# Kernel tuning notes

Measured on AMD Instinct MI355X. Metric: run time of the kernel, lower is better.

## Reference

```python
import jax, jax.numpy as jnp
import numpy as np
from jax import lax

DIM = 256
NUM_HEADS = 8
HEAD_DIM = DIM // NUM_HEADS          # 32
KEY_DIM = int(HEAD_DIM * 0.5)        # 16
SCALE = KEY_DIM ** -0.5
H_QKV = DIM + KEY_DIM * NUM_HEADS * 2  # 512
BN_EPS = 1e-3  # keras BatchNormalization default epsilon


def conv_bn(x, w, gamma, beta, mean, var, groups=1):
    # Conv2D (no bias) + BatchNorm (inference), activation=None
    y = lax.conv_general_dilated(
        x, w, window_strides=(1, 1), padding='SAME',
        dimension_numbers=('NHWC', 'HWIO', 'NHWC'),
        feature_group_count=groups)
    return gamma * (y - mean) * lax.rsqrt(var + BN_EPS) + beta


def setup_inputs() -> dict:
    key = jax.random.key(0)
    ks = jax.random.split(key, 4)
    B, Hs, Ws = 8, 32, 32
    inp = {
        'inputs': jax.random.normal(ks[0], (B, Hs, Ws, DIM), dtype=jnp.float32),
        # qkv: 1x1 conv dim -> h
        'qkv_w': jax.random.normal(ks[1], (1, 1, DIM, H_QKV), dtype=jnp.float32) * 0.05,
        'qkv_gamma': jnp.ones((H_QKV,), jnp.float32),
        'qkv_beta': jnp.zeros((H_QKV,), jnp.float32),
        'qkv_mean': jnp.zeros((H_QKV,), jnp.float32),
        'qkv_var': jnp.ones((H_QKV,), jnp.float32),
        # pe: 3x3 depthwise conv (groups=dim)
        'pe_w': jax.random.normal(ks[2], (3, 3, 1, DIM), dtype=jnp.float32) * 0.05,
        'pe_gamma': jnp.ones((DIM,), jnp.float32),
        'pe_beta': jnp.zeros((DIM,), jnp.float32),
        'pe_mean': jnp.zeros((DIM,), jnp.float32),
        'pe_var': jnp.ones((DIM,), jnp.float32),
        # proj: 1x1 conv dim -> dim
        'proj_w': jax.random.normal(ks[3], (1, 1, DIM, DIM), dtype=jnp.float32) * 0.05,
        'proj_gamma': jnp.ones((DIM,), jnp.float32),
        'proj_beta': jnp.zeros((DIM,), jnp.float32),
        'proj_mean': jnp.zeros((DIM,), jnp.float32),
        'proj_var': jnp.ones((DIM,), jnp.float32),
    }
    return inp


def reference(inputs, qkv_w, qkv_gamma, qkv_beta, qkv_mean, qkv_var,
              pe_w, pe_gamma, pe_beta, pe_mean, pe_var,
              proj_w, proj_gamma, proj_beta, proj_mean, proj_var):
    B, Hs, Ws, C = inputs.shape
    N = Hs * Ws
    x = conv_bn(inputs, qkv_w, qkv_gamma, qkv_beta, qkv_mean, qkv_var)  # [B,H,W,h]
    x = x.reshape(B, N, NUM_HEADS, 2 * KEY_DIM + HEAD_DIM)
    q = x[..., :KEY_DIM]                          # [B,N,nh,kd]
    k = x[..., KEY_DIM:2 * KEY_DIM]               # [B,N,nh,kd]
    v = x[..., 2 * KEY_DIM:]                      # [B,N,nh,hd]
    # attn = q^T @ k^T : [B,nh,N,N]
    attn = jnp.einsum('bnhk,bmhk->bhnm', q, k) * SCALE
    attn = jax.nn.softmax(attn, axis=-1)
    # x = v^T @ attn : [B,nh,hd,N]
    x = jnp.einsum('bnhd,bhnm->bhdm', v, attn)
    # faithful to source: transpose [0,2,1,3] -> [B,hd,nh,N], then reshape NHWC
    x = jnp.transpose(x, (0, 2, 1, 3)).reshape(B, Hs, Ws, C)
    pe = conv_bn(v.reshape(B, Hs, Ws, C), pe_w, pe_gamma, pe_beta, pe_mean, pe_var, groups=C)
    x = x + pe
    x = conv_bn(x, proj_w, proj_gamma, proj_beta, proj_mean, proj_var)
    return x
```

## Files before the change

### kernel.cpp

```cpp
#include <hip/hip_runtime.h>

typedef _Float16 h4 __attribute__((ext_vector_type(4)));
typedef _Float16 h8 __attribute__((ext_vector_type(8)));
typedef float    f4 __attribute__((ext_vector_type(4)));

#define QSCALE (0.25f * 1.44269504088896f)

__device__ __forceinline__ float ex2(float x){ return __builtin_amdgcn_exp2f(x); }

__global__ __launch_bounds__(256) void prep_k(
    const float* __restrict__ X,
    const float* __restrict__ qkvw, const float* __restrict__ qg, const float* __restrict__ qb,
    const float* __restrict__ qm,   const float* __restrict__ qv,
    const float* __restrict__ pew,  const float* __restrict__ pg, const float* __restrict__ pb,
    const float* __restrict__ pm,   const float* __restrict__ pv,
    const float* __restrict__ prw,  const float* __restrict__ prg, const float* __restrict__ prb,
    const float* __restrict__ prm,  const float* __restrict__ prv,
    _Float16* __restrict__ Xh, _Float16* __restrict__ Wqkv, float* __restrict__ bqkv,
    _Float16* __restrict__ Wproj, float* __restrict__ bproj,
    float* __restrict__ peW, float* __restrict__ peB)
{
  const int gid = blockIdx.x*256 + threadIdx.x;
  const int gsz = gridDim.x*256;
  for (int i = gid; i < 2097152/4; i += gsz){
    const float4 xv = ((const float4*)X)[i];
    h4 o; o[0]=(_Float16)xv.x; o[1]=(_Float16)xv.y; o[2]=(_Float16)xv.z; o[3]=(_Float16)xv.w;
    ((h4*)Xh)[i] = o;
  }
  for (int i = gid; i < 512*256; i += gsz){
    int o = i >> 8, c = i & 255;
    float s = qg[o] * rsqrtf(qv[o] + 1e-3f);
    Wqkv[i] = (_Float16)(qkvw[c*512 + o] * s);
  }
  for (int i = gid; i < 512; i += gsz){
    float s = qg[i] * rsqrtf(qv[i] + 1e-3f);
    bqkv[i] = qb[i] - qm[i]*s;
  }
  for (int i = gid; i < 256*256; i += gsz){
    int o = i >> 8, c = i & 255;
    float s = prg[o] * rsqrtf(prv[o] + 1e-3f);
    Wproj[i] = (_Float16)(prw[c*256 + o] * s);
  }
  for (int i = gid; i < 256; i += gsz){
    float s = prg[i] * rsqrtf(prv[i] + 1e-3f);
    bproj[i] = prb[i] - prm[i]*s;
  }
  for (int i = gid; i < 9*256; i += gsz){
    int c = i & 255;
    float s = pg[c] * rsqrtf(pv[c] + 1e-3f);
    peW[i] = pew[i] * s;
  }
  for (int i = gid; i < 256; i += gsz){
    float s = pg[i] * rsqrtf(pv[i] + 1e-3f);
    peB[i] = pb[i] - pm[i]*s;
  }
}

template<int EPI, int MT>
__global__ __launch_bounds__(256) void gemm_staged_k(
    const _Float16* __restrict__ A, const _Float16* __restrict__ Bt,
    const float* __restrict__ bias,
    _Float16* __restrict__ Qh, _Float16* __restrict__ Kh, _Float16* __restrict__ Vh,
    float* __restrict__ Out)
{
  constexpr int BM = MT*32;
  constexpr int AR = BM/64;
  __shared__ __align__(16) _Float16 As[BM*40];
  __shared__ __align__(16) _Float16 Bs[64*40];
  const int t = threadIdx.x, lane = t & 63, wv = t >> 6;
  const int l15 = lane & 15, q = lane >> 4;
  const int wr = wv & 1, wc = wv >> 1;
  const int m0 = blockIdx.x*BM, n0 = blockIdx.y*64;
  const int r4 = t >> 2, s4 = t & 3;
  uint4 ar[AR], br;
  #pragma unroll
  for (int i = 0; i < AR; ++i)
    ar[i] = *(const uint4*)(A + (size_t)(m0 + r4 + i*64)*256 + s4*8);
  br = *(const uint4*)(Bt + (size_t)(n0 + r4)*256 + s4*8);
  f4 acc[MT][2] = {};
  #pragma unroll
  for (int kk = 0; kk < 8; ++kk){
    #pragma unroll
    for (int i = 0; i < AR; ++i)
      *(uint4*)&As[(r4 + i*64)*40 + s4*8] = ar[i];
    *(uint4*)&Bs[r4*40 + s4*8] = br;
    __syncthreads();
    if (kk < 7){
      #pragma unroll
      for (int i = 0; i < AR; ++i)
        ar[i] = *(const uint4*)(A + (size_t)(m0 + r4 + i*64)*256 + (kk+1)*32 + s4*8);
      br = *(const uint4*)(Bt + (size_t)(n0 + r4)*256 + (kk+1)*32 + s4*8);
    }
    #pragma unroll
    for (int mi = 0; mi < MT; ++mi){
      h8 af = *(const h8*)&As[(wr*(MT*16) + mi*16 + l15)*40 + q*8];
      #pragma unroll
      for (int nj = 0; nj < 2; ++nj){
        h8 bf = *(const h8*)&Bs[(wc*32 + nj*16 + l15)*40 + q*8];
        acc[mi][nj] = __builtin_amdgcn_mfma_f32_16x16x32_f16(af, bf, acc[mi][nj], 0,0,0);
      }
    }
    __syncthreads();
  }
  #pragma unroll
  for (int mi = 0; mi < MT; ++mi)
  #pragma unroll
  for (int nj = 0; nj < 2; ++nj){
    const int og = n0 + wc*32 + nj*16 + l15;
    const float bs = bias[og];
    #pragma unroll
    for (int r = 0; r < 4; ++r){
      const int mg = m0 + wr*(MT*16) + mi*16 + q*4 + r;
      const float v = acc[mi][nj][r] + bs;
      if (EPI == 0){
        const int h = og >> 6, j = og & 63;
        const int b = mg >> 10, n = mg & 1023;
        const size_t bhn = (size_t)(b*8+h)*1024 + n;
        if (j < 16)      Qh[bhn*16 + j]      = (_Float16)(v * QSCALE);
        else if (j < 32) Kh[bhn*16 + (j-16)] = (_Float16)v;
        else             Vh[bhn*32 + (j-32)] = (_Float16)v;
      } else {
        Out[(size_t)mg*256 + og] = v;
      }
    }
  }
}

__global__ __launch_bounds__(256) void pass1_k(
    const _Float16* __restrict__ Qh, const _Float16* __restrict__ Kh,
    const _Float16* __restrict__ Vh, _Float16* __restrict__ Vs)
{
  __shared__ __align__(16) _Float16 Ks[64*24];
  const int t = threadIdx.x, lane = t & 63, wv = t >> 6;
  const int l15 = lane & 15, q = lane >> 4;
  const int bh = blockIdx.y;
  const int n0 = (blockIdx.x*4 + wv) * 32;
  const size_t qb = (size_t)bh*1024;
  const h4 af0 = *(const h4*)(Qh + (qb + n0 + l15)*16 + q*4);
  const h4 af1 = *(const h4*)(Qh + (qb + n0 + 16 + l15)*16 + q*4);
  f4 sm0 = {0.f,0.f,0.f,0.f}, sm1 = {0.f,0.f,0.f,0.f};
  const _Float16* kp = Kh + qb*16;
  const int sr = t >> 1, ss = t & 1;
  uint4 kr;
  if (t < 128) kr = *(const uint4*)(kp + sr*16 + ss*8);
  for (int mt = 0; mt < 1024; mt += 64){
    if (t < 128) *(uint4*)&Ks[sr*24 + ss*8] = kr;
    __syncthreads();
    if (t < 128 && mt + 64 < 1024)
      kr = *(const uint4*)(kp + (mt + 64 + sr)*16 + ss*8);
    #pragma unroll
    for (int sub = 0; sub < 4; ++sub){
      h4 bf = *(const h4*)&Ks[(sub*16 + l15)*24 + q*4];
      f4 z = {0.f,0.f,0.f,0.f};
      f4 d0 = __builtin_amdgcn_mfma_f32_16x16x16f16(af0, bf, z, 0,0,0);
      f4 d1 = __builtin_amdgcn_mfma_f32_16x16x16f16(af1, bf, z, 0,0,0);
      #pragma unroll
      for (int r = 0; r < 4; ++r){ sm0[r] += ex2(d0[r]); sm1[r] += ex2(d1[r]); }
    }
    __syncthreads();
  }
  #pragma unroll
  for (int st = 1; st < 16; st <<= 1){
    #pragma unroll
    for (int r = 0; r < 4; ++r){
      sm0[r] += __shfl_xor(sm0[r], st, 64);
      sm1[r] += __shfl_xor(sm1[r], st, 64);
    }
  }
  f4 cv0, cv1;
  #pragma unroll
  for (int r = 0; r < 4; ++r){ cv0[r] = 1.0f/sm0[r]; cv1[r] = 1.0f/sm1[r]; }
  #pragma unroll
  for (int half = 0; half < 2; ++half){
    const int dd = l15 + half*16;
    h4 o0, o1;
    #pragma unroll
    for (int r = 0; r < 4; ++r){
      o0[r] = (_Float16)((float)Vh[(qb + n0 + q*4 + r)*32 + dd] * cv0[r]);
      o1[r] = (_Float16)((float)Vh[(qb + n0 + 16 + q*4 + r)*32 + dd] * cv1[r]);
    }
    *(h4*)(Vs + ((size_t)bh*32 + dd)*1024 + n0 + q*4)      = o0;
    *(h4*)(Vs + ((size_t)bh*32 + dd)*1024 + n0 + 16 + q*4) = o1;
  }
}

__global__ __launch_bounds__(256) void pass2_k(
    const _Float16* __restrict__ Qh, const _Float16* __restrict__ Kh,
    const _Float16* __restrict__ Vs, _Float16* __restrict__ X1h)
{
  __shared__ __align__(16) _Float16 Qs[64*24];
  __shared__ __align__(16) _Float16 Vss[32*72];
  __shared__ float Tt[4][32*33];
  const int t = threadIdx.x, lane = t & 63, wv = t >> 6;
  const int l15 = lane & 15, q = lane >> 4;
  const int bh = blockIdx.y;
  const int b  = bh >> 3, h = bh & 7;
  const int mb = (blockIdx.x*4 + wv) * 32;
  const size_t qb = (size_t)bh*1024;
  const h4 kf0 = *(const h4*)(Kh + (qb + mb + l15)*16 + q*4);
  const h4 kf1 = *(const h4*)(Kh + (qb + mb + 16 + l15)*16 + q*4);
  const _Float16* qp = Qh + qb*16;
  const _Float16* vp = Vs + (size_t)bh*32*1024;
  const int sr = t >> 1, ss = t & 1;
  const int vd = t >> 3, vc = (t & 7)*8;
  uint4 qr, vr;
  if (t < 128) qr = *(const uint4*)(qp + sr*16 + ss*8);
  vr = *(const uint4*)(vp + (size_t)vd*1024 + vc);
  f4 a00={0.f,0.f,0.f,0.f}, a01={0.f,0.f,0.f,0.f};
  f4 a10={0.f,0.f,0.f,0.f}, a11={0.f,0.f,0.f,0.f};
  for (int nt = 0; nt < 1024; nt += 64){
    if (t < 128) *(uint4*)&Qs[sr*24 + ss*8] = qr;
    *(uint4*)&Vss[vd*72 + vc] = vr;
    __syncthreads();
    if (nt + 64 < 1024){
      if (t < 128) qr = *(const uint4*)(qp + (nt + 64 + sr)*16 + ss*8);
      vr = *(const uint4*)(vp + (size_t)vd*1024 + nt + 64 + vc);
    }
    #pragma unroll
    for (int sub = 0; sub < 4; ++sub){
      h4 qf = *(const h4*)&Qs[(sub*16 + l15)*24 + q*4];
      h4 b0 = *(const h4*)&Vss[l15*72      + sub*16 + q*4];
      h4 b1 = *(const h4*)&Vss[(16+l15)*72 + sub*16 + q*4];
      f4 z = {0.f,0.f,0.f,0.f};
      f4 s0 = __builtin_amdgcn_mfma_f32_16x16x16f16(qf, kf0, z, 0,0,0);
      f4 s1 = __builtin_amdgcn_mfma_f32_16x16x16f16(qf, kf1, z, 0,0,0);
      h4 p0, p1;
      #pragma unroll
      for (int r = 0; r < 4; ++r){ p0[r] = (_Float16)ex2(s0[r]); p1[r] = (_Float16)ex2(s1[r]); }
      a00 = __builtin_amdgcn_mfma_f32_16x16x16f16(p0, b0, a00, 0,0,0);
      a01 = __builtin_amdgcn_mfma_f32_16x16x16f16(p0, b1, a01, 0,0,0);
      a10 = __builtin_amdgcn_mfma_f32_16x16x16f16(p1, b0, a10, 0,0,0);
      a11 = __builtin_amdgcn_mfma_f32_16x16x16f16(p1, b1, a11, 0,0,0);
    }
    __syncthreads();
  }
  #pragma unroll
  for (int r = 0; r < 4; ++r){
    Tt[wv][(q*4 + r)*33      + l15]      = a00[r];
    Tt[wv][(q*4 + r)*33      + 16 + l15] = a01[r];
    Tt[wv][(16 + q*4 + r)*33 + l15]      = a10[r];
    Tt[wv][(16 + q*4 + r)*33 + 16 + l15] = a11[r];
  }
  __syncthreads();
  _Float16* xb = X1h + (size_t)b*262144 + (size_t)h*1024 + mb;
  const int mloc = lane & 31, dh = lane >> 5;
  #pragma unroll
  for (int r = 0; r < 16; ++r){
    const int d = r*2 + dh;
    xb[(size_t)d*8192 + mloc] = (_Float16)Tt[wv][mloc*33 + d];
  }
}

__global__ __launch_bounds__(256) void pe_add_k(
    const _Float16* __restrict__ Vh, const _Float16* __restrict__ X1h,
    const float* __restrict__ peW, const float* __restrict__ peB,
    _Float16* __restrict__ X2h)
{
  const int u = blockIdx.x*256 + threadIdx.x;
  const int c0 = (u & 31) * 8;
  const int tok = u >> 5;
  const int b = tok >> 10, n = tok & 1023;
  const int hs = n >> 5, ws = n & 31;
  const int h = c0 >> 5, d0 = c0 & 31;
  const size_t idx8 = (size_t)tok*256 + c0;
  float acc[8];
  {
    f4 b0v = *(const f4*)(peB + c0), b1v = *(const f4*)(peB + c0 + 4);
    #pragma unroll
    for (int j = 0; j < 4; ++j){ acc[j] = b0v[j]; acc[4+j] = b1v[j]; }
  }
  const _Float16* vb = Vh + (size_t)(b*8 + h)*32768 + d0;
  #pragma unroll
  for (int dy = 0; dy < 3; ++dy){
    const int y = hs + dy - 1;
    if ((unsigned)y < 32u){
      #pragma unroll
      for (int dx = 0; dx < 3; ++dx){
        const int x = ws + dx - 1;
        if ((unsigned)x < 32u){
          const int kk = dy*3 + dx;
          h8 vv = *(const h8*)(vb + (size_t)(y*32 + x)*32);
          f4 w0 = *(const f4*)(peW + kk*256 + c0);
          f4 w1 = *(const f4*)(peW + kk*256 + c0 + 4);
          #pragma unroll
          for (int j = 0; j < 4; ++j){
            acc[j]   += w0[j] * (float)vv[j];
            acc[4+j] += w1[j] * (float)vv[4+j];
          }
        }
      }
    }
  }
  h8 x1 = *(const h8*)(X1h + idx8);
  h8 o;
  #pragma unroll
  for (int j = 0; j < 8; ++j) o[j] = (_Float16)((float)x1[j] + acc[j]);
  *(h8*)(X2h + idx8) = o;
}

extern "C" void kernel_launch(void* const* d_in, const int* in_sizes, int n_in,
                              void* d_out, int out_size, void* d_ws, size_t ws_size,
                              hipStream_t stream)
{
  const float* X    = (const float*)d_in[0];
  const float* qkvw = (const float*)d_in[1];
  const float* qg   = (const float*)d_in[2];
  const float* qb   = (const float*)d_in[3];
  const float* qm   = (const float*)d_in[4];
  const float* qv   = (const float*)d_in[5];
  const float* pew  = (const float*)d_in[6];
  const float* pg   = (const float*)d_in[7];
  const float* pb   = (const float*)d_in[8];
  const float* pm   = (const float*)d_in[9];
  const float* pv   = (const float*)d_in[10];
  const float* prw  = (const float*)d_in[11];
  const float* prg  = (const float*)d_in[12];
  const float* prb  = (const float*)d_in[13];
  const float* prm  = (const float*)d_in[14];
  const float* prv  = (const float*)d_in[15];

  char* ws = (char*)d_ws;
  _Float16* Xh    = (_Float16*)(ws + 0);
  _Float16* X2h   = (_Float16*)(ws + 0);
  _Float16* Qh    = (_Float16*)(ws + 4194304);
  _Float16* Kh    = (_Float16*)(ws + 6291456);
  _Float16* Vh    = (_Float16*)(ws + 8388608);
  _Float16* Vs    = (_Float16*)(ws + 12582912);
  _Float16* X1h   = (_Float16*)(ws + 16777216);
  _Float16* Wqkv  = (_Float16*)(ws + 20971520);
  float*    bqkv  = (float*)   (ws + 21233664);
  _Float16* Wproj = (_Float16*)(ws + 21235712);
  float*    bproj = (float*)   (ws + 21366784);
  float*    peW   = (float*)   (ws + 21367808);
  float*    peB   = (float*)   (ws + 21377024);

  prep_k<<<512, 256, 0, stream>>>(X, qkvw, qg, qb, qm, qv, pew, pg, pb, pm, pv,
                                  prw, prg, prb, prm, prv,
                                  Xh, Wqkv, bqkv, Wproj, bproj, peW, peB);
  gemm_staged_k<0,4><<<dim3(64, 8), 256, 0, stream>>>(Xh, Wqkv, bqkv,
                                                      Qh, Kh, Vh, nullptr);
  pass1_k<<<dim3(8, 64), 256, 0, stream>>>(Qh, Kh, Vh, Vs);
  pass2_k<<<dim3(8, 64), 256, 0, stream>>>(Qh, Kh, Vs, X1h);
  pe_add_k<<<1024, 256, 0, stream>>>(Vh, X1h, peW, peB, X2h);
  gemm_staged_k<1,2><<<dim3(128, 4), 256, 0, stream>>>(X2h, Wproj, bproj,
                                                       nullptr, nullptr, nullptr,
                                                       (float*)d_out);
}
```

Baseline: 150.8 us.

## Fuse input fp16 cast into QKV GEMM and stage whole K/Q per block

The fp32-to-fp16 conversion of the input moves out of the prep kernel and into a new QKV GEMM that loads fp32 X directly, removing a full write and re-read of the converted activations. Both GEMMs become 64x64 tiles with two 128-wide K chunks, in place of eight 32-wide steps. pass1 now loads all 1024 keys for a head into shared memory once, so the per-tile barriers go away. pass2 preloads all Q into LDS and streams V in 256-column chunks. The cost is much larger shared-memory use per block (about 40-57 KB), which may lower occupancy.

```diff
diff --git a/kernel.cpp b/kernel.cpp
--- a/kernel.cpp
+++ b/kernel.cpp
@@ -9,24 +9,18 @@
 __device__ __forceinline__ float ex2(float x){ return __builtin_amdgcn_exp2f(x); }
 
 __global__ __launch_bounds__(256) void prep_k(
-    const float* __restrict__ X,
     const float* __restrict__ qkvw, const float* __restrict__ qg, const float* __restrict__ qb,
     const float* __restrict__ qm,   const float* __restrict__ qv,
     const float* __restrict__ pew,  const float* __restrict__ pg, const float* __restrict__ pb,
     const float* __restrict__ pm,   const float* __restrict__ pv,
     const float* __restrict__ prw,  const float* __restrict__ prg, const float* __restrict__ prb,
     const float* __restrict__ prm,  const float* __restrict__ prv,
-    _Float16* __restrict__ Xh, _Float16* __restrict__ Wqkv, float* __restrict__ bqkv,
+    _Float16* __restrict__ Wqkv, float* __restrict__ bqkv,
     _Float16* __restrict__ Wproj, float* __restrict__ bproj,
     float* __restrict__ peW, float* __restrict__ peB)
 {
   const int gid = blockIdx.x*256 + threadIdx.x;
   const int gsz = gridDim.x*256;
-  for (int i = gid; i < 2097152/4; i += gsz){
-    const float4 xv = ((const float4*)X)[i];
-    h4 o; o[0]=(_Float16)xv.x; o[1]=(_Float16)xv.y; o[2]=(_Float16)xv.z; o[3]=(_Float16)xv.w;
-    ((h4*)Xh)[i] = o;
-  }
   for (int i = gid; i < 512*256; i += gsz){
     int o = i >> 8, c = i & 255;
     float s = qg[o] * rsqrtf(qv[o] + 1e-3f);
@@ -56,72 +50,156 @@
   }
 }
 
-template<int EPI, int MT>
-__global__ __launch_bounds__(256) void gemm_staged_k(
-    const _Float16* __restrict__ A, const _Float16* __restrict__ Bt,
+__global__ __launch_bounds__(256) void qkv_gemm_k(
+    const float* __restrict__ X, const _Float16* __restrict__ Wqkv,
     const float* __restrict__ bias,
-    _Float16* __restrict__ Qh, _Float16* __restrict__ Kh, _Float16* __restrict__ Vh,
-    float* __restrict__ Out)
-{
-  constexpr int BM = MT*32;
-  constexpr int AR = BM/64;
-  __shared__ __align__(16) _Float16 As[BM*40];
-  __shared__ __align__(16) _Float16 Bs[64*40];
+    _Float16* __restrict__ Qh, _Float16* __restrict__ Kh, _Float16* __restrict__ Vh)
+{
+  __shared__ __align__(16) _Float16 As[64*136];
+  __shared__ __align__(16) _Float16 Bs[64*136];
   const int t = threadIdx.x, lane = t & 63, wv = t >> 6;
   const int l15 = lane & 15, q = lane >> 4;
   const int wr = wv & 1, wc = wv >> 1;
-  const int m0 = blockIdx.x*BM, n0 = blockIdx.y*64;
-  const int r4 = t >> 2, s4 = t & 3;
-  uint4 ar[AR], br;
-  #pragma unroll
-  for (int i = 0; i < AR; ++i)
-    ar[i] = *(const uint4*)(A + (size_t)(m0 + r4 + i*64)*256 + s4*8);
-  br = *(const uint4*)(Bt + (size_t)(n0 + r4)*256 + s4*8);
-  f4 acc[MT][2] = {};
-  #pragma unroll
-  for (int kk = 0; kk < 8; ++kk){
-    #pragma unroll
-    for (int i = 0; i < AR; ++i)
-      *(uint4*)&As[(r4 + i*64)*40 + s4*8] = ar[i];
-    *(uint4*)&Bs[r4*40 + s4*8] = br;
-    __syncthreads();
-    if (kk < 7){
-      #pragma unroll
-      for (int i = 0; i < AR; ++i)
-        ar[i] = *(const uint4*)(A + (size_t)(m0 + r4 + i*64)*256 + (kk+1)*32 + s4*8);
-      br = *(const uint4*)(Bt + (size_t)(n0 + r4)*256 + (kk+1)*32 + s4*8);
-    }
-    #pragma unroll
-    for (int mi = 0; mi < MT; ++mi){
-      h8 af = *(const h8*)&As[(wr*(MT*16) + mi*16 + l15)*40 + q*8];
-      #pragma unroll
-      for (int nj = 0; nj < 2; ++nj){
-        h8 bf = *(const h8*)&Bs[(wc*32 + nj*16 + l15)*40 + q*8];
-        acc[mi][nj] = __builtin_amdgcn_mfma_f32_16x16x32_f16(af, bf, acc[mi][nj], 0,0,0);
+  const int m0 = blockIdx.x*64, n0 = blockIdx.y*64;
+  const int ar = t >> 2, ac = t & 3;
+  float4 av[8]; uint4 bv[4];
+  #pragma unroll
+  for (int i = 0; i < 8; ++i){
+    int idx = i*256 + t, row = idx >> 5, c4 = idx & 31;
+    av[i] = *(const float4*)(X + (size_t)(m0+row)*256 + c4*4);
+  }
+  #pragma unroll
+  for (int i = 0; i < 4; ++i){
+    int idx = i*256 + t, row = idx >> 4, seg = idx & 15;
+    bv[i] = *(const uint4*)(Wqkv + (size_t)(n0+row)*256 + seg*8);
+  }
+  f4 acc[2][2] = {};
+  #pragma unroll
+  for (int kc = 0; kc < 2; ++kc){
+    #pragma unroll
+    for (int i = 0; i < 8; ++i){
+      int idx = i*256 + t, row = idx >> 5, c4 = idx & 31;
+      h4 o; o[0]=(_Float16)av[i].x; o[1]=(_Float16)av[i].y;
+            o[2]=(_Float16)av[i].z; o[3]=(_Float16)av[i].w;
+      *(h4*)&As[row*136 + c4*4] = o;
+    }
+    #pragma unroll
+    for (int i = 0; i < 4; ++i){
+      int idx = i*256 + t, row = idx >> 4, seg = idx & 15;
+      *(uint4*)&Bs[row*136 + seg*8] = bv[i];
+    }
+    __syncthreads();
+    if (kc == 0){
+      #pragma unroll
+      for (int i = 0; i < 8; ++i){
+        int idx = i*256 + t, row = idx >> 5, c4 = idx & 31;
+        av[i] = *(const float4*)(X + (size_t)(m0+row)*256 + 128 + c4*4);
       }
-    }
-    __syncthreads();
-  }
-  #pragma unroll
-  for (int mi = 0; mi < MT; ++mi)
+      #pragma unroll
+      for (int i = 0; i < 4; ++i){
+        int idx = i*256 + t, row = idx >> 4, seg = idx & 15;
+        bv[i] = *(const uint4*)(Wqkv + (size_t)(n0+row)*256 + 128 + seg*8);
+      }
+    }
+    #pragma unroll
+    for (int kk = 0; kk < 4; ++kk){
+      h8 af[2], bf[2];
+      #pragma unroll
+      for (int mi = 0; mi < 2; ++mi)
+        af[mi] = *(const h8*)&As[(wr*32 + mi*16 + l15)*136 + kk*32 + q*8];
+      #pragma unroll
+      for (int nj = 0; nj < 2; ++nj)
+        bf[nj] = *(const h8*)&Bs[(wc*32 + nj*16 + l15)*136 + kk*32 + q*8];
+      #pragma unroll
+      for (int mi = 0; mi < 2; ++mi)
+      #pragma unroll
+      for (int nj = 0; nj < 2; ++nj)
+        acc[mi][nj] = __builtin_amdgcn_mfma_f32_16x16x32_f16(af[mi], bf[nj], acc[mi][nj], 0,0,0);
+    }
+    __syncthreads();
+  }
+  #pragma unroll
+  for (int mi = 0; mi < 2; ++mi)
+  #pragma unroll
+  for (int nj = 0; nj < 2; ++nj){
+    const int og = n0 + wc*32 + nj*16 + l15;
+    const int h = og >> 6, j = og & 63;
+    const float bs = bias[og];
+    #pragma unroll
+    for (int r = 0; r < 4; ++r){
+      const int mg = m0 + wr*32 + mi*16 + q*4 + r;
+      const int b = mg >> 10, n = mg & 1023;
+      const size_t bhn = (size_t)(b*8+h)*1024 + n;
+      const float v = acc[mi][nj][r] + bs;
+      if (j < 16)      Qh[bhn*16 + j]      = (_Float16)(v * QSCALE);
+      else if (j < 32) Kh[bhn*16 + (j-16)] = (_Float16)v;
+      else             Vh[bhn*32 + (j-32)] = (_Float16)v;
+    }
+  }
+}
+
+__global__ __launch_bounds__(256) void proj_gemm_k(
+    const _Float16* __restrict__ A, const _Float16* __restrict__ Wproj,
+    const float* __restrict__ bias, float* __restrict__ Out)
+{
+  __shared__ __align__(16) _Float16 As[64*136];
+  __shared__ __align__(16) _Float16 Bs[64*136];
+  const int t = threadIdx.x, lane = t & 63, wv = t >> 6;
+  const int l15 = lane & 15, q = lane >> 4;
+  const int wr = wv & 1, wc = wv >> 1;
+  const int m0 = blockIdx.x*64, n0 = blockIdx.y*64;
+  uint4 av[4], bv[4];
+  #pragma unroll
+  for (int i = 0; i < 4; ++i){
+    int idx = i*256 + t, row = idx >> 4, seg = idx & 15;
+    av[i] = *(const uint4*)(A     + (size_t)(m0+row)*256 + seg*8);
+    bv[i] = *(const uint4*)(Wproj + (size_t)(n0+row)*256 + seg*8);
+  }
+  f4 acc[2][2] = {};
+  #pragma unroll
+  for (int kc = 0; kc < 2; ++kc){
+    #pragma unroll
+    for (int i = 0; i < 4; ++i){
+      int idx = i*256 + t, row = idx >> 4, seg = idx & 15;
+      *(uint4*)&As[row*136 + seg*8] = av[i];
+      *(uint4*)&Bs[row*136 + seg*8] = bv[i];
+    }
+    __syncthreads();
+    if (kc == 0){
+      #pragma unroll
+      for (int i = 0; i < 4; ++i){
+        int idx = i*256 + t, row = idx >> 4, seg = idx & 15;
+        av[i] = *(const uint4*)(A     + (size_t)(m0+row)*256 + 128 + seg*8);
+        bv[i] = *(const uint4*)(Wproj + (size_t)(n0+row)*256 + 128 + seg*8);
+      }
+    }
+    #pragma unroll
+    for (int kk = 0; kk < 4; ++kk){
+      h8 af[2], bf[2];
+      #pragma unroll
+      for (int mi = 0; mi < 2; ++mi)
+        af[mi] = *(const h8*)&As[(wr*32 + mi*16 + l15)*136 + kk*32 + q*8];
+      #pragma unroll
+      for (int nj = 0; nj < 2; ++nj)
+        bf[nj] = *(const h8*)&Bs[(wc*32 + nj*16 + l15)*136 + kk*32 + q*8];
+      #pragma unroll
+      for (int mi = 0; mi < 2; ++mi)
+      #pragma unroll
+      for (int nj = 0; nj < 2; ++nj)
+        acc[mi][nj] = __builtin_amdgcn_mfma_f32_16x16x32_f16(af[mi], bf[nj], acc[mi][nj], 0,0,0);
+    }
+    __syncthreads();
+  }
+  #pragma unroll
+  for (int mi = 0; mi < 2; ++mi)
   #pragma unroll
   for (int nj = 0; nj < 2; ++nj){
     const int og = n0 + wc*32 + nj*16 + l15;
     const float bs = bias[og];
     #pragma unroll
     for (int r = 0; r < 4; ++r){
-      const int mg = m0 + wr*(MT*16) + mi*16 + q*4 + r;
-      const float v = acc[mi][nj][r] + bs;
-      if (EPI == 0){
-        const int h = og >> 6, j = og & 63;
-        const int b = mg >> 10, n = mg & 1023;
-        const size_t bhn = (size_t)(b*8+h)*1024 + n;
-        if (j < 16)      Qh[bhn*16 + j]      = (_Float16)(v * QSCALE);
-        else if (j < 32) Kh[bhn*16 + (j-16)] = (_Float16)v;
-        else             Vh[bhn*32 + (j-32)] = (_Float16)v;
-      } else {
-        Out[(size_t)mg*256 + og] = v;
-      }
+      const int mg = m0 + wr*32 + mi*16 + q*4 + r;
+      Out[(size_t)mg*256 + og] = acc[mi][nj][r] + bs;
     }
   }
 }
@@ -130,34 +208,30 @@
     const _Float16* __restrict__ Qh, const _Float16* __restrict__ Kh,
     const _Float16* __restrict__ Vh, _Float16* __restrict__ Vs)
 {
-  __shared__ __align__(16) _Float16 Ks[64*24];
+  __shared__ __align__(16) _Float16 Ks[1024*20];
   const int t = threadIdx.x, lane = t & 63, wv = t >> 6;
   const int l15 = lane & 15, q = lane >> 4;
   const int bh = blockIdx.y;
-  const int n0 = (blockIdx.x*4 + wv) * 32;
+  const int n0 = blockIdx.x*128 + wv*32;
   const size_t qb = (size_t)bh*1024;
+  const _Float16* kp = Kh + qb*16;
+  #pragma unroll
+  for (int i = 0; i < 8; ++i){
+    int idx = i*256 + t, row = idx >> 1, seg = idx & 1;
+    *(uint4*)&Ks[row*20 + seg*8] = *(const uint4*)(kp + row*16 + seg*8);
+  }
   const h4 af0 = *(const h4*)(Qh + (qb + n0 + l15)*16 + q*4);
   const h4 af1 = *(const h4*)(Qh + (qb + n0 + 16 + l15)*16 + q*4);
+  __syncthreads();
   f4 sm0 = {0.f,0.f,0.f,0.f}, sm1 = {0.f,0.f,0.f,0.f};
-  const _Float16* kp = Kh + qb*16;
-  const int sr = t >> 1, ss = t & 1;
-  uint4 kr;
-  if (t < 128) kr = *(const uint4*)(kp + sr*16 + ss*8);
-  for (int mt = 0; mt < 1024; mt += 64){
-    if (t < 128) *(uint4*)&Ks[sr*24 + ss*8] = kr;
-    __syncthreads();
-    if (t < 128 && mt + 64 < 1024)
-      kr = *(const uint4*)(kp + (mt + 64 + sr)*16 + ss*8);
-    #pragma unroll
-    for (int sub = 0; sub < 4; ++sub){
-      h4 bf = *(const h4*)&Ks[(sub*16 + l15)*24 + q*4];
-      f4 z = {0.f,0.f,0.f,0.f};
-      f4 d0 = __builtin_amdgcn_mfma_f32_16x16x16f16(af0, bf, z, 0,0,0);
-      f4 d1 = __builtin_amdgcn_mfma_f32_16x16x16f16(af1, bf, z, 0,0,0);
-      #pragma unroll
-      for (int r = 0; r < 4; ++r){ sm0[r] += ex2(d0[r]); sm1[r] += ex2(d1[r]); }
-    }
-    __syncthreads();
+  #pragma unroll 8
+  for (int mt = 0; mt < 64; ++mt){
+    h4 bf = *(const h4*)&Ks[(mt*16 + l15)*20 + q*4];
+    f4 z = {0.f,0.f,0.f,0.f};
+    f4 d0 = __builtin_amdgcn_mfma_f32_16x16x16f16(af0, bf, z, 0,0,0);
+    f4 d1 = __builtin_amdgcn_mfma_f32_16x16x16f16(af1, bf, z, 0,0,0);
+    #pragma unroll
+    for (int r = 0; r < 4; ++r){ sm0[r] += ex2(d0[r]); sm1[r] += ex2(d1[r]); }
   }
   #pragma unroll
   for (int st = 1; st < 16; st <<= 1){
@@ -188,39 +262,53 @@
     const _Float16* __restrict__ Qh, const _Float16* __restrict__ Kh,
     const _Float16* __restrict__ Vs, _Float16* __restrict__ X1h)
 {
-  __shared__ __align__(16) _Float16 Qs[64*24];
-  __shared__ __align__(16) _Float16 Vss[32*72];
-  __shared__ float Tt[4][32*33];
+  __shared__ __align__(16) char smem[1024*20*2 + 32*264*2];
+  _Float16* Qs  = (_Float16*)smem;
+  _Float16* Vss = (_Float16*)(smem + 40960);
+  float*    Tt  = (float*)smem;
   const int t = threadIdx.x, lane = t & 63, wv = t >> 6;
   const int l15 = lane & 15, q = lane >> 4;
   const int bh = blockIdx.y;
   const int b  = bh >> 3, h = bh & 7;
-  const int mb = (blockIdx.x*4 + wv) * 32;
+  const int mb = blockIdx.x*128 + wv*32;
   const size_t qb = (size_t)bh*1024;
   const h4 kf0 = *(const h4*)(Kh + (qb + mb + l15)*16 + q*4);
   const h4 kf1 = *(const h4*)(Kh + (qb + mb + 16 + l15)*16 + q*4);
   const _Float16* qp = Qh + qb*16;
   const _Float16* vp = Vs + (size_t)bh*32*1024;
-  const int sr = t >> 1, ss = t & 1;
-  const int vd = t >> 3, vc = (t & 7)*8;
-  uint4 qr, vr;
-  if (t < 128) qr = *(const uint4*)(qp + sr*16 + ss*8);
-  vr = *(const uint4*)(vp + (size_t)vd*1024 + vc);
+  #pragma unroll
+  for (int i = 0; i < 8; ++i){
+    int idx = i*256 + t, row = idx >> 1, seg = idx & 1;
+    *(uint4*)&Qs[row*20 + seg*8] = *(const uint4*)(qp + row*16 + seg*8);
+  }
+  uint4 vr[4];
+  #pragma unroll
+  for (int i = 0; i < 4; ++i){
+    int idx = i*256 + t, d = idx >> 5, seg = idx & 31;
+    vr[i] = *(const uint4*)(vp + (size_t)d*1024 + seg*8);
+  }
   f4 a00={0.f,0.f,0.f,0.f}, a01={0.f,0.f,0.f,0.f};
   f4 a10={0.f,0.f,0.f,0.f}, a11={0.f,0.f,0.f,0.f};
-  for (int nt = 0; nt < 1024; nt += 64){
-    if (t < 128) *(uint4*)&Qs[sr*24 + ss*8] = qr;
-    *(uint4*)&Vss[vd*72 + vc] = vr;
-    __syncthreads();
-    if (nt + 64 < 1024){
-      if (t < 128) qr = *(const uint4*)(qp + (nt + 64 + sr)*16 + ss*8);
-      vr = *(const uint4*)(vp + (size_t)vd*1024 + nt + 64 + vc);
-    }
-    #pragma unroll
-    for (int sub = 0; sub < 4; ++sub){
-      h4 qf = *(const h4*)&Qs[(sub*16 + l15)*24 + q*4];
-      h4 b0 = *(const h4*)&Vss[l15*72      + sub*16 + q*4];
-      h4 b1 = *(const h4*)&Vss[(16+l15)*72 + sub*16 + q*4];
+  for (int c = 0; c < 4; ++c){
+    const int nt = c*256;
+    #pragma unroll
+    for (int i = 0; i < 4; ++i){
+      int idx = i*256 + t, d = idx >> 5, seg = idx & 31;
+      *(uint4*)&Vss[d*264 + seg*8] = vr[i];
+    }
+    __syncthreads();
+    if (c < 3){
+      #pragma unroll
+      for (int i = 0; i < 4; ++i){
+        int idx = i*256 + t, d = idx >> 5, seg = idx & 31;
+        vr[i] = *(const uint4*)(vp + (size_t)d*1024 + nt + 256 + seg*8);
+      }
+    }
+    #pragma unroll 4
+    for (int sub = 0; sub < 16; ++sub){
+      h4 qf = *(const h4*)&Qs[(nt + sub*16 + l15)*20 + q*4];
+      h4 b0 = *(const h4*)&Vss[l15*264      + sub*16 + q*4];
+      h4 b1 = *(const h4*)&Vss[(16+l15)*264 + sub*16 + q*4];
       f4 z = {0.f,0.f,0.f,0.f};
       f4 s0 = __builtin_amdgcn_mfma_f32_16x16x16f16(qf, kf0, z, 0,0,0);
       f4 s1 = __builtin_amdgcn_mfma_f32_16x16x16f16(qf, kf1, z, 0,0,0);
@@ -234,12 +322,13 @@
     }
     __syncthreads();
   }
+  float* tw = Tt + wv*(32*33);
   #pragma unroll
   for (int r = 0; r < 4; ++r){
-    Tt[wv][(q*4 + r)*33      + l15]      = a00[r];
-    Tt[wv][(q*4 + r)*33      + 16 + l15] = a01[r];
-    Tt[wv][(16 + q*4 + r)*33 + l15]      = a10[r];
-    Tt[wv][(16 + q*4 + r)*33 + 16 + l15] = a11[r];
+    tw[(q*4 + r)*33      + l15]      = a00[r];
+    tw[(q*4 + r)*33      + 16 + l15] = a01[r];
+    tw[(16 + q*4 + r)*33 + l15]      = a10[r];
+    tw[(16 + q*4 + r)*33 + 16 + l15] = a11[r];
   }
   __syncthreads();
   _Float16* xb = X1h + (size_t)b*262144 + (size_t)h*1024 + mb;
@@ -247,7 +336,7 @@
   #pragma unroll
   for (int r = 0; r < 16; ++r){
     const int d = r*2 + dh;
-    xb[(size_t)d*8192 + mloc] = (_Float16)Tt[wv][mloc*33 + d];
+    xb[(size_t)d*8192 + mloc] = (_Float16)tw[mloc*33 + d];
   }
 }
 
@@ -320,7 +409,6 @@
   const float* prv  = (const float*)d_in[15];
 
   char* ws = (char*)d_ws;
-  _Float16* Xh    = (_Float16*)(ws + 0);
   _Float16* X2h   = (_Float16*)(ws + 0);
   _Float16* Qh    = (_Float16*)(ws + 4194304);
   _Float16* Kh    = (_Float16*)(ws + 6291456);
@@ -334,15 +422,12 @@
   float*    peW   = (float*)   (ws + 21367808);
   float*    peB   = (float*)   (ws + 21377024);
 
-  prep_k<<<512, 256, 0, stream>>>(X, qkvw, qg, qb, qm, qv, pew, pg, pb, pm, pv,
-                                  prw, prg, prb, prm, prv,
-                                  Xh, Wqkv, bqkv, Wproj, bproj, peW, peB);
-  gemm_staged_k<0,4><<<dim3(64, 8), 256, 0, stream>>>(Xh, Wqkv, bqkv,
-                                                      Qh, Kh, Vh, nullptr);
+  prep_k<<<64, 256, 0, stream>>>(qkvw, qg, qb, qm, qv, pew, pg, pb, pm, pv,
+                                 prw, prg, prb, prm, prv,
+                                 Wqkv, bqkv, Wproj, bproj, peW, peB);
+  qkv_gemm_k<<<dim3(128, 8), 256, 0, stream>>>(X, Wqkv, bqkv, Qh, Kh, Vh);
   pass1_k<<<dim3(8, 64), 256, 0, stream>>>(Qh, Kh, Vh, Vs);
   pass2_k<<<dim3(8, 64), 256, 0, stream>>>(Qh, Kh, Vs, X1h);
   pe_add_k<<<1024, 256, 0, stream>>>(Vh, X1h, peW, peB, X2h);
-  gemm_staged_k<1,2><<<dim3(128, 4), 256, 0, stream>>>(X2h, Wproj, bproj,
-                                                       nullptr, nullptr, nullptr,
-                                                       (float*)d_out);
-}
+  proj_gemm_k<<<dim3(128, 4), 256, 0, stream>>>(X2h, Wproj, bproj, (float*)d_out);
+}
```

Result: slower. 185.7 us (+23.2%).
